# Kernel optimization log

Measured on AMD Instinct MI355X. Metric: run time of the kernel, lower is better.

Reference implementation:

```python
import math
import jax, jax.numpy as jnp
import numpy as np

WIN = 8
NUM_HEADS = 8

def _rel_pos_index(win):
    coords = np.stack(np.meshgrid(np.arange(win), np.arange(win), indexing='ij'))
    cf = coords.reshape(2, -1)
    rel = cf[:, :, None] - cf[:, None, :]
    rel = rel.transpose(1, 2, 0).copy()
    rel[:, :, 0] += win - 1
    rel[:, :, 1] += win - 1
    rel[:, :, 0] *= 2 * win - 1
    return rel.sum(-1)  # [N, N]

def _shift_mask(H, W, win, Ho, Wo):
    m = np.zeros((H, W))
    h_slices = (slice(0, -win), slice(-win, -Ho), slice(-Ho, None)) if Ho > 0 else (slice(0, None),)
    w_slices = (slice(0, -win), slice(-win, -Wo), slice(-Wo, None)) if Wo > 0 else (slice(0, None),)
    cnt = 0
    for hs in h_slices:
        for ws in w_slices:
            m[hs, ws] = cnt
            cnt += 1
    mw = m.reshape(H // win, win, W // win, win).transpose(0, 2, 1, 3).reshape(-1, win * win)
    d = mw[:, None, :] - mw[:, :, None]
    return np.where(d != 0, -100.0, 0.0).astype(np.float32)  # [nW, N, N]

def _ln(x, g, b, eps=1e-5):
    mu = jnp.mean(x, axis=-1, keepdims=True)
    var = jnp.mean((x - mu) ** 2, axis=-1, keepdims=True)
    return (x - mu) / jnp.sqrt(var + eps) * g + b

def _win_part(x, win):
    B, H, W, C = x.shape
    x = x.reshape(B, H // win, win, W // win, win, C).transpose(0, 1, 3, 2, 4, 5)
    return x.reshape(-1, win * win, C)

def _win_rev(w, win, H, W):
    C = w.shape[-1]
    B = w.shape[0] // ((H // win) * (W // win))
    x = w.reshape(B, H // win, W // win, win, win, C).transpose(0, 1, 3, 2, 4, 5)
    return x.reshape(B, H, W, C)

def setup_inputs() -> dict:
    key = jax.random.key(0)
    ks = jax.random.split(key, 10)
    B, L, C, hid = 4, 32768, 256, 1024
    s = 0.02
    return {
        'x': jax.random.normal(ks[0], (B, L, C), jnp.float32),
        'norm1_g': jnp.ones((C,), jnp.float32),
        'norm1_b': jnp.zeros((C,), jnp.float32),
        'wq': jax.random.normal(ks[1], (C, C), jnp.float32) * s,
        'bq': jnp.zeros((C,), jnp.float32),
        'wv': jax.random.normal(ks[2], (C, C), jnp.float32) * s,
        'bv': jnp.zeros((C,), jnp.float32),
        'rpb': jax.random.normal(ks[3], (225, NUM_HEADS), jnp.float32) * s,
        'wproj': jax.random.normal(ks[4], (C, C), jnp.float32) * s,
        'bproj': jnp.zeros((C,), jnp.float32),
        'norm2_g': jnp.ones((C,), jnp.float32),
        'norm2_b': jnp.zeros((C,), jnp.float32),
        'w1': jax.random.normal(ks[5], (C, hid), jnp.float32) * s,
        'b1': jnp.zeros((hid,), jnp.float32),
        'dw_k': jax.random.normal(ks[6], (hid, 1, 3, 3), jnp.float32) * s,
        'dw_b': jnp.zeros((hid,), jnp.float32),
        'w2': jax.random.normal(ks[7], (hid, C), jnp.float32) * s,
        'b2': jnp.zeros((C,), jnp.float32),
        'H_offset': 3,
        'W_offset': 5,
    }

def reference(x, norm1_g, norm1_b, wq, bq, wv, bv, rpb, wproj, bproj,
              norm2_g, norm2_b, w1, b1, dw_k, dw_b, w2, b2, H_offset, W_offset):
    B, L, C = x.shape
    H = int(round(math.sqrt(L * 2)))
    W = int(round(math.sqrt(L // 2)))
    win, h = WIN, NUM_HEADS
    hd = C // h
    N = win * win
    nW = (H // win) * (W // win)
    scale = hd ** -0.5

    shortcut = x
    xn = _ln(x, norm1_g, norm1_b)
    q = xn @ wq + bq
    v = xn @ wv + bv
    q = q.reshape(B, H, W, C)
    v = v.reshape(B, H, W, C)
    k = q  # module uses k = q (shared)

    q = jnp.roll(q, (-H_offset, -W_offset), axis=(1, 2))
    k = jnp.roll(k, (-H_offset, -W_offset), axis=(1, 2))
    v = jnp.roll(v, (-H_offset, -W_offset), axis=(1, 2))

    qw = _win_part(q, win).reshape(-1, N, h, hd).transpose(0, 2, 1, 3)
    kw = _win_part(k, win).reshape(-1, N, h, hd).transpose(0, 2, 1, 3)
    vw = _win_part(v, win).reshape(-1, N, h, hd).transpose(0, 2, 1, 3)

    attn = jnp.einsum('bhnd,bhmd->bhnm', qw * scale, kw)
    bias = rpb[jnp.asarray(_rel_pos_index(win).reshape(-1))].reshape(N, N, h).transpose(2, 0, 1)
    attn = attn + bias[None]
    mask = jnp.asarray(_shift_mask(H, W, win, int(H_offset), int(W_offset)))
    attn = (attn.reshape(B, nW, h, N, N) + mask[None, :, None]).reshape(-1, h, N, N)
    attn = jax.nn.softmax(attn, axis=-1)

    y = jnp.einsum('bhnm,bhmd->bhnd', attn, vw).transpose(0, 2, 1, 3).reshape(-1, N, C)
    y = y @ wproj + bproj
    y = _win_rev(y.reshape(-1, win, win, C), win, H, W)
    y = jnp.roll(y, (H_offset, W_offset), axis=(1, 2)).reshape(B, L, C)

    x = shortcut + y

    # LeFF
    xn2 = _ln(x, norm2_g, norm2_b)
    t = jax.nn.gelu(xn2 @ w1 + b1, approximate=False)  # [B, L, hid]
    t = t.reshape(B, H, W, -1).transpose(0, 3, 1, 2)   # NCHW
    t = jax.lax.conv_general_dilated(t, dw_k, (1, 1), 'SAME',
                                     feature_group_count=t.shape[1],
                                     dimension_numbers=('NCHW', 'OIHW', 'NCHW'))
    t = jax.nn.gelu(t + dw_b[None, :, None, None], approximate=False)
    t = t.transpose(0, 2, 3, 1).reshape(B, L, -1)
    t = t @ w2 + b2
    return x + t
```

## Files before the change

kernel.cpp:

```cpp
#include <hip/hip_runtime.h>
#include <stdint.h>
#include <math.h>

#define H_IMG 256
#define W_IMG 128
#define LTOK  32768
#define BATCH 4
#define CDIM  256
#define HIDDIM 1024
#define NHEAD 8
#define HD    32
#define MROWS 131072

typedef __attribute__((ext_vector_type(8))) short short8;
typedef __attribute__((ext_vector_type(4))) float f32x4;

__device__ __forceinline__ float bf2f(unsigned u) {
  union { unsigned u; float f; } c; c.u = u << 16; return c.f;
}
__device__ __forceinline__ unsigned short f2bf(float f) {
  union { float f; unsigned u; } c; c.f = f;
  unsigned r = c.u + 0x7fffu + ((c.u >> 16) & 1u);
  return (unsigned short)(r >> 16);
}
__device__ __forceinline__ void unpack8(uint4 t, float* dst) {
  dst[0] = bf2f(t.x & 0xffffu); dst[1] = bf2f(t.x >> 16);
  dst[2] = bf2f(t.y & 0xffffu); dst[3] = bf2f(t.y >> 16);
  dst[4] = bf2f(t.z & 0xffffu); dst[5] = bf2f(t.z >> 16);
  dst[6] = bf2f(t.w & 0xffffu); dst[7] = bf2f(t.w >> 16);
}
__device__ __forceinline__ float gelu_f(float x) {
  return 0.5f * x * (1.0f + erff(x * 0.70710678118654752f));
}
__device__ __forceinline__ void gload_lds16(const void* g, void* l) {
  __builtin_amdgcn_global_load_lds(
      (const __attribute__((address_space(1))) unsigned int*)g,
      (__attribute__((address_space(3))) unsigned int*)l, 16, 0, 0);
}

__global__ __launch_bounds__(256) void wconv_kernel(
    const float* __restrict__ w, unsigned short* __restrict__ wt, int K, int N) {
  __shared__ float t[32][33];
  const int k0 = blockIdx.x * 32, n0 = blockIdx.y * 32;
  const int tx = threadIdx.x & 31, ty = threadIdx.x >> 5;
#pragma unroll
  for (int i = 0; i < 4; ++i)
    t[ty + 8 * i][tx] = w[(size_t)(k0 + ty + 8 * i) * N + n0 + tx];
  __syncthreads();
#pragma unroll
  for (int i = 0; i < 4; ++i)
    wt[(size_t)(n0 + ty + 8 * i) * K + k0 + tx] = f2bf(t[tx][ty + 8 * i]);
}

__global__ __launch_bounds__(256) void ln_kernel(
    const float* __restrict__ x, const float* __restrict__ g,
    const float* __restrict__ b, unsigned short* __restrict__ out) {
  const int wave = threadIdx.x >> 6;
  const int lane = threadIdx.x & 63;
  const size_t row = (size_t)blockIdx.x * 4 + wave;
  float4 f = ((const float4*)(x + row * CDIM))[lane];
  float s  = f.x + f.y + f.z + f.w;
  float sq = f.x*f.x + f.y*f.y + f.z*f.z + f.w*f.w;
#pragma unroll
  for (int o = 32; o > 0; o >>= 1) { s += __shfl_down(s, o); sq += __shfl_down(sq, o); }
  s = __shfl(s, 0); sq = __shfl(sq, 0);
  const float mu = s * (1.0f / CDIM);
  const float var = sq * (1.0f / CDIM) - mu * mu;
  const float rstd = rsqrtf(var + 1e-5f);
  float4 gg = ((const float4*)g)[lane];
  float4 bb = ((const float4*)b)[lane];
  unsigned short o4[4];
  o4[0] = f2bf((f.x - mu) * rstd * gg.x + bb.x);
  o4[1] = f2bf((f.y - mu) * rstd * gg.y + bb.y);
  o4[2] = f2bf((f.z - mu) * rstd * gg.z + bb.z);
  o4[3] = f2bf((f.w - mu) * rstd * gg.w + bb.w);
  *(uint2*)(out + row * CDIM + lane * 4) = *(uint2*)o4;
}

template<int EPI>
__global__ __launch_bounds__(256) void mgemm(
    const unsigned short* __restrict__ A, const unsigned short* __restrict__ Bt,
    const float* __restrict__ bias, float bscale, const float* __restrict__ res,
    void* __restrict__ outp, int K, int ldc) {
  __shared__ unsigned short As[128][32];
  __shared__ unsigned short Bs[128][32];
  const int tid = threadIdx.x;
  const int w = tid >> 6, lane = tid & 63;
  const int m0 = blockIdx.x * 128, n0 = blockIdx.y * 128;
  const int wm = (w & 1) * 64, wn = (w >> 1) * 64;
  const int srow = lane >> 2;
  const int csrc = (lane & 3) ^ (srow & 3);
  f32x4 acc[4][4];
#pragma unroll
  for (int mi = 0; mi < 4; ++mi)
#pragma unroll
    for (int ni = 0; ni < 4; ++ni)
#pragma unroll
      for (int r = 0; r < 4; ++r) acc[mi][ni][r] = 0.0f;

  const int kg = lane >> 4, ml = lane & 15;
  for (int kk = 0; kk < K; kk += 32) {
#pragma unroll
    for (int i = 0; i < 2; ++i) {
      const int rl = w * 32 + i * 16 + srow;
      gload_lds16(A + (size_t)(m0 + rl) * K + kk + csrc * 8, &As[w * 32 + i * 16][0]);
      gload_lds16(Bt + (size_t)(n0 + rl) * K + kk + csrc * 8, &Bs[w * 32 + i * 16][0]);
    }
    __syncthreads();
    short8 af[4], bg[4];
#pragma unroll
    for (int mi = 0; mi < 4; ++mi) {
      const int r = wm + mi * 16 + ml;
      af[mi] = *(const short8*)&As[r][(kg ^ (r & 3)) * 8];
    }
#pragma unroll
    for (int ni = 0; ni < 4; ++ni) {
      const int r = wn + ni * 16 + ml;
      bg[ni] = *(const short8*)&Bs[r][(kg ^ (r & 3)) * 8];
    }
#pragma unroll
    for (int mi = 0; mi < 4; ++mi)
#pragma unroll
      for (int ni = 0; ni < 4; ++ni)
        acc[mi][ni] = __builtin_amdgcn_mfma_f32_16x16x32_bf16(af[mi], bg[ni], acc[mi][ni], 0, 0, 0);
    __syncthreads();
  }
#pragma unroll
  for (int ni = 0; ni < 4; ++ni) {
    const int n = n0 + wn + ni * 16 + ml;
    const float bn = bias[n] * bscale;
#pragma unroll
    for (int mi = 0; mi < 4; ++mi) {
#pragma unroll
      for (int r = 0; r < 4; ++r) {
        const int m = m0 + wm + mi * 16 + kg * 4 + r;
        const size_t idx = (size_t)m * ldc + n;
        float val = acc[mi][ni][r] + bn;
        if (EPI == 1) {
          ((float*)outp)[idx] = val + res[idx];
        } else if (EPI == 2) {
          ((unsigned short*)outp)[idx] = f2bf(gelu_f(val));
        } else {
          ((unsigned short*)outp)[idx] = f2bf(val);
        }
      }
    }
  }
}

__global__ __launch_bounds__(64) void attn_kernel(
    const unsigned short* __restrict__ q, const unsigned short* __restrict__ v,
    const float* __restrict__ rpb, const int* __restrict__ pHo,
    const int* __restrict__ pWo, unsigned short* __restrict__ yout) {
  __shared__ unsigned short qs[64][32];
  __shared__ unsigned short vs[64][32];
  __shared__ float bias_s[225];
  __shared__ int reg_s[64];
  const int lane = threadIdx.x;
  const int hh = blockIdx.y;
  const int wb = blockIdx.x;
  const int b = wb >> 9, wloc = wb & 511;
  const int wh = wloc >> 4, ww = wloc & 15;
  const int Ho = pHo[0], Wo = pWo[0];
  const int dy = lane >> 3, dx = lane & 7;
  const int hr = wh * 8 + dy, wr = ww * 8 + dx;
  int ho = hr + Ho; if (ho >= H_IMG) ho -= H_IMG;
  int wo = wr + Wo; if (wo >= W_IMG) wo -= W_IMG;
  const size_t base = ((size_t)b * LTOK + (size_t)ho * W_IMG + wo) * CDIM + hh * HD;

  float qr[32];
  const uint4* qp = (const uint4*)(q + base);
  const uint4* vp = (const uint4*)(v + base);
#pragma unroll
  for (int u = 0; u < 4; ++u) {
    uint4 t = qp[u];
    *(uint4*)&qs[lane][u * 8] = t;
    unpack8(t, &qr[u * 8]);
    *(uint4*)&vs[lane][u * 8] = vp[u];
  }
  const int rh = (hr < H_IMG - 8) ? 0 : ((hr < H_IMG - Ho) ? 1 : 2);
  const int rw = (wr < W_IMG - 8) ? 0 : ((wr < W_IMG - Wo) ? 1 : 2);
  reg_s[lane] = rh * 3 + rw;
  for (int i = lane; i < 225; i += 64) bias_s[i] = rpb[i * 8 + hh];
  __syncthreads();

  const float scale = 0.17677669529663687f;
#pragma unroll
  for (int k2 = 0; k2 < 32; ++k2) qr[k2] *= scale;

  float p[64];
  float mx = -3.0e38f;
  const int myreg = reg_s[lane];
#pragma unroll
  for (int j = 0; j < 64; ++j) {
    float s = 0.0f;
#pragma unroll
    for (int u = 0; u < 4; ++u) {
      float f8[8];
      unpack8(*(const uint4*)&qs[j][u * 8], f8);
#pragma unroll
      for (int e = 0; e < 8; ++e) s += qr[u * 8 + e] * f8[e];
    }
    const int rel = (dy - (j >> 3) + 7) * 15 + (dx - (j & 7) + 7);
    s += bias_s[rel];
    if (reg_s[j] != myreg) s -= 100.0f;
    p[j] = s;
    mx = fmaxf(mx, s);
  }
  float sum = 0.0f;
#pragma unroll
  for (int j = 0; j < 64; ++j) { float e = __expf(p[j] - mx); p[j] = e; sum += e; }
  const float inv = 1.0f / sum;
  float acc[32] = {};
#pragma unroll
  for (int j = 0; j < 64; ++j) {
    const float pj = p[j] * inv;
#pragma unroll
    for (int u = 0; u < 4; ++u) {
      float f8[8];
      unpack8(*(const uint4*)&vs[j][u * 8], f8);
#pragma unroll
      for (int e = 0; e < 8; ++e) acc[u * 8 + e] += pj * f8[e];
    }
  }
  unsigned short o[32];
#pragma unroll
  for (int k2 = 0; k2 < 32; ++k2) o[k2] = f2bf(acc[k2]);
  uint4* op = (uint4*)(yout + base);
#pragma unroll
  for (int u = 0; u < 4; ++u) op[u] = ((uint4*)o)[u];
}

__global__ __launch_bounds__(256) void dwconv_kernel(
    const unsigned short* __restrict__ t1b, const float* __restrict__ k9,
    const float* __restrict__ bias, unsigned short* __restrict__ t2b,
    int hr0, int band_rows) {
  const int c = blockIdx.y * 128 + (threadIdx.x & 31) * 4;
  const int tok = blockIdx.x * 8 + (threadIdx.x >> 5);
  const int h = hr0 + (tok >> 7), wcol = tok & 127;
  float wreg[4][9];
#pragma unroll
  for (int j = 0; j < 4; ++j)
#pragma unroll
    for (int tp = 0; tp < 9; ++tp) wreg[j][tp] = k9[(c + j) * 9 + tp];
  const float4 bv = *(const float4*)(bias + c);
  float a0 = 0, a1 = 0, a2 = 0, a3 = 0;
#pragma unroll
  for (int ky = 0; ky < 3; ++ky) {
    const int hy = h + ky - 1;
    if ((unsigned)hy >= (unsigned)H_IMG) continue;
    const int brow = (tok >> 7) + ky;
#pragma unroll
    for (int kx = 0; kx < 3; ++kx) {
      const int wx = wcol + kx - 1;
      if ((unsigned)wx >= (unsigned)W_IMG) continue;
      const ushort4 tv = *(const ushort4*)(
          t1b + ((size_t)(brow * 128 + wx)) * HIDDIM + c);
      const int tp = ky * 3 + kx;
      a0 += bf2f(tv.x) * wreg[0][tp];
      a1 += bf2f(tv.y) * wreg[1][tp];
      a2 += bf2f(tv.z) * wreg[2][tp];
      a3 += bf2f(tv.w) * wreg[3][tp];
    }
  }
  a0 = gelu_f(a0 + bv.x); a1 = gelu_f(a1 + bv.y);
  a2 = gelu_f(a2 + bv.z); a3 = gelu_f(a3 + bv.w);
  unsigned short o[4] = { f2bf(a0), f2bf(a1), f2bf(a2), f2bf(a3) };
  *(uint2*)(t2b + (size_t)tok * HIDDIM + c) = *(uint2*)o;
}

extern "C" void kernel_launch(void* const* d_in, const int* in_sizes, int n_in,
                              void* d_out, int out_size, void* d_ws, size_t ws_size,
                              hipStream_t stream) {
  (void)in_sizes; (void)n_in; (void)out_size; (void)ws_size;
  const float* x     = (const float*)d_in[0];
  const float* n1g   = (const float*)d_in[1];
  const float* n1b   = (const float*)d_in[2];
  const float* wq    = (const float*)d_in[3];
  const float* bq    = (const float*)d_in[4];
  const float* wv    = (const float*)d_in[5];
  const float* bv    = (const float*)d_in[6];
  const float* rpb   = (const float*)d_in[7];
  const float* wproj = (const float*)d_in[8];
  const float* bproj = (const float*)d_in[9];
  const float* n2g   = (const float*)d_in[10];
  const float* n2b   = (const float*)d_in[11];
  const float* w1    = (const float*)d_in[12];
  const float* b1    = (const float*)d_in[13];
  const float* dwk   = (const float*)d_in[14];
  const float* dwb   = (const float*)d_in[15];
  const float* w2    = (const float*)d_in[16];
  const float* b2    = (const float*)d_in[17];
  const int*   pHo   = (const int*)d_in[18];
  const int*   pWo   = (const int*)d_in[19];
  float* out = (float*)d_out;

  char* wsb = (char*)d_ws;
  unsigned short* r0     = (unsigned short*)wsb;
  unsigned short* wqt    = (unsigned short*)(wsb + 67108864ull);
  unsigned short* wvt    = (unsigned short*)(wsb + 67108864ull + 131072ull);
  unsigned short* wprojt = (unsigned short*)(wsb + 67108864ull + 262144ull);
  unsigned short* w1t    = (unsigned short*)(wsb + 67108864ull + 393216ull);
  unsigned short* w2t    = (unsigned short*)(wsb + 67108864ull + 917504ull);
  unsigned short* t1b    = (unsigned short*)(wsb + 68550656ull);
  unsigned short* t2b    = (unsigned short*)(wsb + 68550656ull + 25690112ull);
  unsigned short* vb     = (unsigned short*)d_out;
  unsigned short* qb     = (unsigned short*)((char*)d_out + 67108864ull);

  wconv_kernel<<<dim3(8, 8),  256, 0, stream>>>(wq,    wqt,    CDIM, CDIM);
  wconv_kernel<<<dim3(8, 8),  256, 0, stream>>>(wv,    wvt,    CDIM, CDIM);
  wconv_kernel<<<dim3(8, 8),  256, 0, stream>>>(wproj, wprojt, CDIM, CDIM);
  wconv_kernel<<<dim3(8, 32), 256, 0, stream>>>(w1,    w1t,    CDIM, HIDDIM);
  wconv_kernel<<<dim3(32, 8), 256, 0, stream>>>(w2,    w2t,    HIDDIM, CDIM);

  ln_kernel<<<32768, 256, 0, stream>>>(x, n1g, n1b, r0);
  mgemm<0><<<dim3(1024, 2), 256, 0, stream>>>(r0, wqt, bq, 1.0f, nullptr, qb, CDIM, CDIM);
  mgemm<0><<<dim3(1024, 2), 256, 0, stream>>>(r0, wvt, bv, 1.0f, nullptr, vb, CDIM, CDIM);
  attn_kernel<<<dim3(2048, NHEAD), 64, 0, stream>>>(qb, vb, rpb, pHo, pWo, r0);
  mgemm<1><<<dim3(1024, 2), 256, 0, stream>>>(r0, wprojt, bproj, 1.0f, x, out, CDIM, CDIM);
  ln_kernel<<<32768, 256, 0, stream>>>(out, n2g, n2b, r0);
  for (int bi = 0; bi < BATCH; ++bi) {
    for (int hr0 = 0; hr0 < H_IMG; ) {
      const int br = (H_IMG - hr0 >= 96) ? 96 : (H_IMG - hr0);
      const int r_start = (hr0 > 0) ? hr0 - 1 : 0;
      const int r_end = (hr0 + br <= H_IMG - 1) ? hr0 + br : H_IMG - 1;
      const int nrows = r_end - r_start + 1;
      const unsigned short* Aff1 = r0 + ((size_t)bi * LTOK + (size_t)r_start * W_IMG) * CDIM;
      unsigned short* t1dst = t1b + (size_t)(r_start - hr0 + 1) * W_IMG * HIDDIM;
      mgemm<2><<<dim3(nrows, 8), 256, 0, stream>>>(
          Aff1, w1t, b1, 1.0f, nullptr, t1dst, CDIM, HIDDIM);
      dwconv_kernel<<<dim3(br * 16, 8), 256, 0, stream>>>(t1b, dwk, dwb, t2b, hr0, br);
      const size_t btok = (size_t)bi * LTOK + (size_t)hr0 * W_IMG;
      mgemm<1><<<dim3(br, 2), 256, 0, stream>>>(
          t2b, w2t, b2, 1.0f, out + btok * CDIM, out + btok * CDIM, HIDDIM, CDIM);
      hr0 += br;
    }
  }
}
```

Before: 1.941 ms.

## Rewrite window attention to use MFMA bf16 with four heads per block

Moves the window attention from scalar per-lane dot products to MFMA 16x16x32 bf16 matrix ops for both QK^T and PV. Each 256-thread block now handles one window with each wave processing two heads. Q is loaded straight to LDS via global_load_lds, V is transposed in LDS, and the softmax uses cross-lane shuffles with a swizzled bf16 P buffer. The mask is applied only on edge windows. The aim is to remove the heavy VALU and register cost of the scalar path, at the price of rounding probabilities to bf16 and more complex LDS indexing.

```diff
diff --git a/kernel.cpp b/kernel.cpp
--- a/kernel.cpp
+++ b/kernel.cpp
@@ -22,12 +22,6 @@
   union { float f; unsigned u; } c; c.f = f;
   unsigned r = c.u + 0x7fffu + ((c.u >> 16) & 1u);
   return (unsigned short)(r >> 16);
-}
-__device__ __forceinline__ void unpack8(uint4 t, float* dst) {
-  dst[0] = bf2f(t.x & 0xffffu); dst[1] = bf2f(t.x >> 16);
-  dst[2] = bf2f(t.y & 0xffffu); dst[3] = bf2f(t.y >> 16);
-  dst[4] = bf2f(t.z & 0xffffu); dst[5] = bf2f(t.z >> 16);
-  dst[6] = bf2f(t.w & 0xffffu); dst[7] = bf2f(t.w >> 16);
 }
 __device__ __forceinline__ float gelu_f(float x) {
   return 0.5f * x * (1.0f + erff(x * 0.70710678118654752f));
@@ -148,16 +142,16 @@
   }
 }
 
-__global__ __launch_bounds__(64) void attn_kernel(
+__global__ __launch_bounds__(256, 3) void attn_kernel(
     const unsigned short* __restrict__ q, const unsigned short* __restrict__ v,
     const float* __restrict__ rpb, const int* __restrict__ pHo,
     const int* __restrict__ pWo, unsigned short* __restrict__ yout) {
-  __shared__ unsigned short qs[64][32];
-  __shared__ unsigned short vs[64][32];
-  __shared__ float bias_s[225];
+  __shared__ char wbuf[4][8704];
+  __shared__ float bias_w[4][228];
   __shared__ int reg_s[64];
-  const int lane = threadIdx.x;
-  const int hh = blockIdx.y;
+  const int tid = threadIdx.x;
+  const int w = tid >> 6, lane = tid & 63;
+  const int g = lane >> 4, c = lane & 15;
   const int wb = blockIdx.x;
   const int b = wb >> 9, wloc = wb & 511;
   const int wh = wloc >> 4, ww = wloc & 15;
@@ -166,69 +160,147 @@
   const int hr = wh * 8 + dy, wr = ww * 8 + dx;
   int ho = hr + Ho; if (ho >= H_IMG) ho -= H_IMG;
   int wo = wr + Wo; if (wo >= W_IMG) wo -= W_IMG;
-  const size_t base = ((size_t)b * LTOK + (size_t)ho * W_IMG + wo) * CDIM + hh * HD;
-
-  float qr[32];
-  const uint4* qp = (const uint4*)(q + base);
-  const uint4* vp = (const uint4*)(v + base);
-#pragma unroll
-  for (int u = 0; u < 4; ++u) {
-    uint4 t = qp[u];
-    *(uint4*)&qs[lane][u * 8] = t;
-    unpack8(t, &qr[u * 8]);
-    *(uint4*)&vs[lane][u * 8] = vp[u];
-  }
-  const int rh = (hr < H_IMG - 8) ? 0 : ((hr < H_IMG - Ho) ? 1 : 2);
-  const int rw = (wr < W_IMG - 8) ? 0 : ((wr < W_IMG - Wo) ? 1 : 2);
-  reg_s[lane] = rh * 3 + rw;
-  for (int i = lane; i < 225; i += 64) bias_s[i] = rpb[i * 8 + hh];
+  const size_t tok = (size_t)b * LTOK + (size_t)ho * W_IMG + wo;
+  const bool edge = (wh == (H_IMG / 8 - 1)) || (ww == (W_IMG / 8 - 1));
+  if (w == 0) {
+    const int rh = (hr < H_IMG - 8) ? 0 : ((hr < H_IMG - Ho) ? 1 : 2);
+    const int rw = (wr < W_IMG - 8) ? 0 : ((wr < W_IMG - Wo) ? 1 : 2);
+    reg_s[lane] = rh * 3 + rw;
+  }
   __syncthreads();
 
+  unsigned short* qh = (unsigned short*)&wbuf[w][0];
+  unsigned short* vt = (unsigned short*)&wbuf[w][4096];
+  unsigned short* Pp = (unsigned short*)&wbuf[w][0];
+
   const float scale = 0.17677669529663687f;
-#pragma unroll
-  for (int k2 = 0; k2 < 32; ++k2) qr[k2] *= scale;
-
-  float p[64];
-  float mx = -3.0e38f;
-  const int myreg = reg_s[lane];
-#pragma unroll
-  for (int j = 0; j < 64; ++j) {
-    float s = 0.0f;
+  const int dxk = c & 7, dyk0 = c >> 3;
+  const int base_l = 112 - dyk0 * 15 - dxk;
+
+  for (int p2 = 0; p2 < 2; ++p2) {
+    const int hh = w + 4 * p2;
+    const uint4* vp = (const uint4*)(v + tok * CDIM + hh * HD);
+    uint4 a0 = vp[0], a1 = vp[1], a2 = vp[2], a3 = vp[3];
+#pragma unroll
+    for (int i = 0; i < 4; ++i) {
+      const int idx = lane + 64 * i;
+      if (idx < 225) bias_w[w][idx] = rpb[idx * 8 + hh];
+    }
 #pragma unroll
     for (int u = 0; u < 4; ++u) {
-      float f8[8];
-      unpack8(*(const uint4*)&qs[j][u * 8], f8);
-#pragma unroll
-      for (int e = 0; e < 8; ++e) s += qr[u * 8 + e] * f8[e];
-    }
-    const int rel = (dy - (j >> 3) + 7) * 15 + (dx - (j & 7) + 7);
-    s += bias_s[rel];
-    if (reg_s[j] != myreg) s -= 100.0f;
-    p[j] = s;
-    mx = fmaxf(mx, s);
-  }
-  float sum = 0.0f;
-#pragma unroll
-  for (int j = 0; j < 64; ++j) { float e = __expf(p[j] - mx); p[j] = e; sum += e; }
-  const float inv = 1.0f / sum;
-  float acc[32] = {};
-#pragma unroll
-  for (int j = 0; j < 64; ++j) {
-    const float pj = p[j] * inv;
-#pragma unroll
-    for (int u = 0; u < 4; ++u) {
-      float f8[8];
-      unpack8(*(const uint4*)&vs[j][u * 8], f8);
-#pragma unroll
-      for (int e = 0; e < 8; ++e) acc[u * 8 + e] += pj * f8[e];
-    }
-  }
-  unsigned short o[32];
-#pragma unroll
-  for (int k2 = 0; k2 < 32; ++k2) o[k2] = f2bf(acc[k2]);
-  uint4* op = (uint4*)(yout + base);
-#pragma unroll
-  for (int u = 0; u < 4; ++u) op[u] = ((uint4*)o)[u];
+      const int t2 = u * 16 + (lane >> 2);
+      int ho2 = wh * 8 + (t2 >> 3) + Ho; if (ho2 >= H_IMG) ho2 -= H_IMG;
+      int wo2 = ww * 8 + (t2 & 7) + Wo;  if (wo2 >= W_IMG) wo2 -= W_IMG;
+      const size_t tk = (size_t)b * LTOK + (size_t)ho2 * W_IMG + wo2;
+      gload_lds16(q + tk * CDIM + hh * HD + (lane & 3) * 8, &qh[u * 512]);
+    }
+    {
+      unsigned tmp[16] = {a0.x,a0.y,a0.z,a0.w,a1.x,a1.y,a1.z,a1.w,
+                          a2.x,a2.y,a2.z,a2.w,a3.x,a3.y,a3.z,a3.w};
+#pragma unroll
+      for (int d2 = 0; d2 < 16; ++d2) {
+        vt[(2 * d2) * 72 + lane]     = (unsigned short)(tmp[d2] & 0xffffu);
+        vt[(2 * d2 + 1) * 72 + lane] = (unsigned short)(tmp[d2] >> 16);
+      }
+    }
+    asm volatile("s_waitcnt vmcnt(0)" ::: "memory");
+    short8 q4[4];
+#pragma unroll
+    for (int mi = 0; mi < 4; ++mi)
+      q4[mi] = *(const short8*)&qh[(16 * mi + c) * 32 + g * 8];
+    short8 vf[2][2];
+#pragma unroll
+    for (int s2 = 0; s2 < 2; ++s2)
+#pragma unroll
+      for (int n2 = 0; n2 < 2; ++n2)
+        vf[s2][n2] = *(const short8*)&vt[(16 * n2 + c) * 72 + 32 * s2 + 8 * g];
+    f32x4 acc[4][4];
+#pragma unroll
+    for (int mi = 0; mi < 4; ++mi)
+#pragma unroll
+      for (int nj = 0; nj < 4; ++nj)
+#pragma unroll
+        for (int r = 0; r < 4; ++r) acc[mi][nj][r] = 0.0f;
+#pragma unroll
+    for (int mi = 0; mi < 4; ++mi)
+#pragma unroll
+      for (int nj = 0; nj < 4; ++nj)
+        acc[mi][nj] = __builtin_amdgcn_mfma_f32_16x16x32_bf16(q4[mi], q4[nj], acc[mi][nj], 0, 0, 0);
+    int regk[4];
+    if (edge) {
+#pragma unroll
+      for (int nj = 0; nj < 4; ++nj) regk[nj] = reg_s[16 * nj + c];
+    }
+#pragma unroll
+    for (int mi = 0; mi < 4; ++mi) {
+#pragma unroll
+      for (int r = 0; r < 4; ++r) {
+        const int qq = 16 * mi + 4 * g + r;
+        const int rb = (qq >> 3) * 15 + (qq & 7) + base_l;
+        float sv[4];
+#pragma unroll
+        for (int nj = 0; nj < 4; ++nj)
+          sv[nj] = acc[mi][nj][r] * scale + bias_w[w][rb - 30 * nj];
+        if (edge) {
+          const int regq = reg_s[qq];
+#pragma unroll
+          for (int nj = 0; nj < 4; ++nj)
+            if (regq != regk[nj]) sv[nj] -= 100.0f;
+        }
+        float mx2 = fmaxf(fmaxf(sv[0], sv[1]), fmaxf(sv[2], sv[3]));
+        mx2 = fmaxf(mx2, __shfl_xor(mx2, 1));
+        mx2 = fmaxf(mx2, __shfl_xor(mx2, 2));
+        mx2 = fmaxf(mx2, __shfl_xor(mx2, 4));
+        mx2 = fmaxf(mx2, __shfl_xor(mx2, 8));
+        float e0 = __expf(sv[0] - mx2), e1 = __expf(sv[1] - mx2);
+        float e2 = __expf(sv[2] - mx2), e3 = __expf(sv[3] - mx2);
+        float sm = e0 + e1 + e2 + e3;
+        sm += __shfl_xor(sm, 1);
+        sm += __shfl_xor(sm, 2);
+        sm += __shfl_xor(sm, 4);
+        sm += __shfl_xor(sm, 8);
+        const float iv = __builtin_amdgcn_rcpf(sm);
+        const int rowoff = qq * 64, sw = qq & 7;
+        Pp[rowoff + ((dyk0 ^ sw) * 8)       + dxk] = f2bf(e0 * iv);
+        Pp[rowoff + (((2 + dyk0) ^ sw) * 8) + dxk] = f2bf(e1 * iv);
+        Pp[rowoff + (((4 + dyk0) ^ sw) * 8) + dxk] = f2bf(e2 * iv);
+        Pp[rowoff + (((6 + dyk0) ^ sw) * 8) + dxk] = f2bf(e3 * iv);
+      }
+    }
+    f32x4 oacc[4][2];
+#pragma unroll
+    for (int mi = 0; mi < 4; ++mi)
+#pragma unroll
+      for (int n2 = 0; n2 < 2; ++n2)
+#pragma unroll
+        for (int r = 0; r < 4; ++r) oacc[mi][n2][r] = 0.0f;
+#pragma unroll
+    for (int s2 = 0; s2 < 2; ++s2) {
+      short8 pa[4];
+#pragma unroll
+      for (int mi = 0; mi < 4; ++mi) {
+        const int qq2 = 16 * mi + c;
+        pa[mi] = *(const short8*)&Pp[qq2 * 64 + (((4 * s2 + g) ^ (qq2 & 7)) * 8)];
+      }
+#pragma unroll
+      for (int mi = 0; mi < 4; ++mi)
+#pragma unroll
+        for (int n2 = 0; n2 < 2; ++n2)
+          oacc[mi][n2] = __builtin_amdgcn_mfma_f32_16x16x32_bf16(pa[mi], vf[s2][n2], oacc[mi][n2], 0, 0, 0);
+    }
+    unsigned short* Ost = Pp;
+#pragma unroll
+    for (int mi = 0; mi < 4; ++mi)
+#pragma unroll
+      for (int n2 = 0; n2 < 2; ++n2)
+#pragma unroll
+        for (int r = 0; r < 4; ++r)
+          Ost[(16 * mi + 4 * g + r) * 40 + 16 * n2 + c] = f2bf(oacc[mi][n2][r]);
+    uint4* op = (uint4*)(yout + tok * CDIM + hh * HD);
+#pragma unroll
+    for (int u = 0; u < 4; ++u)
+      op[u] = *(const uint4*)&Ost[lane * 40 + u * 8];
+  }
 }
 
 __global__ __launch_bounds__(256) void dwconv_kernel(
@@ -316,7 +388,7 @@
   ln_kernel<<<32768, 256, 0, stream>>>(x, n1g, n1b, r0);
   mgemm<0><<<dim3(1024, 2), 256, 0, stream>>>(r0, wqt, bq, 1.0f, nullptr, qb, CDIM, CDIM);
   mgemm<0><<<dim3(1024, 2), 256, 0, stream>>>(r0, wvt, bv, 1.0f, nullptr, vb, CDIM, CDIM);
-  attn_kernel<<<dim3(2048, NHEAD), 64, 0, stream>>>(qb, vb, rpb, pHo, pWo, r0);
+  attn_kernel<<<dim3(2048), 256, 0, stream>>>(qb, vb, rpb, pHo, pWo, r0);
   mgemm<1><<<dim3(1024, 2), 256, 0, stream>>>(r0, wprojt, bproj, 1.0f, x, out, CDIM, CDIM);
   ln_kernel<<<32768, 256, 0, stream>>>(out, n2g, n2b, r0);
   for (int bi = 0; bi < BATCH; ++bi) {
```

After: 1.635 ms. -15.7%, faster.
